# Performance work log

Measured on AMD Instinct MI355X. Metric: run time of the kernel, lower is better.

Reference implementation:

```python
import jax, jax.numpy as jnp
import numpy as np

D = 1024      # d_model
H = 16        # n_heads
HD = D // H   # head_dim = 64
B = 2
NQ = 2048     # prod(spatial_shape_q)
NK = 2048     # prod(spatial_shape_kv)
SCALE_BASE_Q = 2 * NQ   # spatial_shape_q[0] * 2
SCALE_BASE_K = 2 * NK   # spatial_shape_kv[0] * 2
THETA = 10000.0         # theta_rescale_factor=1.0 -> theta unchanged


def _init_freqs(dim):
    # learned_freq=True: parameter initialized to standard rotary frequencies
    return 1.0 / (THETA ** (jnp.arange(0, dim, 2, dtype=jnp.float32) / dim))


def _rotate_half(x):
    # interleaved pair rotation: (x1, x2) -> (-x2, x1)
    x1 = x[..., ::2]
    x2 = x[..., 1::2]
    return jnp.stack((-x2, x1), axis=-1).reshape(x.shape)


def _apply_rope_xpos(x, freqs_param, scale_base, sign):
    # x: (B, H, N, HD); freqs_param: (HD//2,)
    n = x.shape[2]
    dim = x.shape[-1]
    t = jnp.arange(n, dtype=jnp.float32)
    freqs = jnp.repeat(t[:, None] * freqs_param[None, :], 2, axis=-1)  # (N, HD)
    # xpos length-extrapolatable scaling
    power = (t - n // 2) / scale_base                                   # (N,)
    sv = (jnp.arange(0, dim, 2, dtype=jnp.float32) + 0.4 * dim) / (1.4 * dim)
    scale = jnp.repeat(sv[None, :] ** power[:, None], 2, axis=-1) ** sign  # (N, HD)
    return x * jnp.cos(freqs) * scale + _rotate_half(x) * jnp.sin(freqs) * scale


def setup_inputs() -> dict:
    key = jax.random.key(0)
    ks = jax.random.split(key, 10)
    s = 0.02
    return {
        "q_seq": jax.random.normal(ks[0], (B, NQ, D), jnp.float32),
        "kv_seq": jax.random.normal(ks[1], (B, NK, D), jnp.float32),
        "Wq": jax.random.normal(ks[2], (D, D), jnp.float32) * s,
        "bq": jnp.zeros((D,), jnp.float32),
        "Wk": jax.random.normal(ks[3], (D, D), jnp.float32) * s,
        "bk": jnp.zeros((D,), jnp.float32),
        "Wv": jax.random.normal(ks[4], (D, D), jnp.float32) * s,
        "bv": jnp.zeros((D,), jnp.float32),
        "Wo": jax.random.normal(ks[5], (D, D), jnp.float32) * s,
        "bo": jnp.zeros((D,), jnp.float32),
        "freqs_q": _init_freqs(HD),
        "freqs_kv": _init_freqs(HD),
    }


def reference(q_seq, kv_seq, Wq, bq, Wk, bk, Wv, bv, Wo, bo, freqs_q, freqs_kv):
    Bq, Nq, C = q_seq.shape
    Nk = kv_seq.shape[1]
    q = (q_seq @ Wq.T + bq).reshape(Bq, Nq, H, HD).transpose(0, 2, 1, 3)
    k = (kv_seq @ Wk.T + bk).reshape(Bq, Nk, H, HD).transpose(0, 2, 1, 3)
    v = (kv_seq @ Wv.T + bv).reshape(Bq, Nk, H, HD).transpose(0, 2, 1, 3)
    q = _apply_rope_xpos(q, freqs_q, SCALE_BASE_Q, sign=1.0)   # queries: scale^{+1}
    k = _apply_rope_xpos(k, freqs_kv, SCALE_BASE_K, sign=-1.0)  # keys: scale^{-1}
    attn = jax.nn.softmax(
        jnp.einsum("bhqd,bhkd->bhqk", q, k) * (HD ** -0.5), axis=-1
    )
    out = jnp.einsum("bhqk,bhkd->bhqd", attn, v)
    out = out.transpose(0, 2, 1, 3).reshape(Bq, Nq, C)
    return (out @ Wo.T + bo, attn)
```

## Files before the change

### kernel.cpp

```cpp
#include <hip/hip_runtime.h>

#define NQ 2048
#define NKK 2048
#define DD 1024
#define HH 16

typedef __attribute__((ext_vector_type(8))) short bf16x8;
typedef __attribute__((ext_vector_type(4))) float f32x4;

__device__ __forceinline__ short f2bf(float f){
    union { float f; unsigned u; } v; v.f = f;
    unsigned u = v.u + 0x7FFFu + ((v.u >> 16) & 1u);
    return (short)(u >> 16);
}
__device__ __forceinline__ float bf2f(unsigned short u){
    union { unsigned u; float f; } v; v.u = ((unsigned)u) << 16;
    return v.f;
}

__device__ __forceinline__ void gload16(const void* g, void* l){
    __builtin_amdgcn_global_load_lds(
        (__attribute__((address_space(1))) void*)g,
        (__attribute__((address_space(3))) void*)l,
        16, 0, 0);
}

__global__ __launch_bounds__(256) void cvt_bf16(const float* __restrict__ src,
                                                short* __restrict__ dst, int n){
    int i = (blockIdx.x * 256 + threadIdx.x) * 4;
    if (i < n){
        float4 v = *(const float4*)(src + i);
        union { short s[4]; uint2 u; } o;
        o.s[0] = f2bf(v.x); o.s[1] = f2bf(v.y);
        o.s[2] = f2bf(v.z); o.s[3] = f2bf(v.w);
        *(uint2*)(dst + i) = o.u;
    }
}

__global__ __launch_bounds__(256) void rope_kernel(const short* __restrict__ x,
                                                   short* __restrict__ y,
                                                   const float* __restrict__ fr,
                                                   int N, float scale_base,
                                                   float sign, float prescale){
    int p = blockIdx.x * 256 + threadIdx.x;
    int col2 = p & 511;
    int row  = p >> 9;
    int n    = row & (N - 1);
    int i    = col2 & 31;
    float t  = (float)n;
    float fv = t * fr[i];
    float c = cosf(fv), s = sinf(fv);
    float power = (t - (float)(N / 2)) / scale_base;
    float sv = ((float)(2 * i) + 0.4f * 64.f) / (1.4f * 64.f);
    float scale = exp2f(sign * power * log2f(sv)) * prescale;
    unsigned xv = *(const unsigned*)(x + 2 * (size_t)p);
    float x0 = bf2f((unsigned short)(xv & 0xFFFFu));
    float x1 = bf2f((unsigned short)(xv >> 16));
    float y0 = (x0 * c - x1 * s) * scale;
    float y1 = (x1 * c + x0 * s) * scale;
    unsigned o = (unsigned)(unsigned short)f2bf(y0) |
                 ((unsigned)(unsigned short)f2bf(y1) << 16);
    *(unsigned*)(y + 2 * (size_t)p) = o;
}

template<bool F32OUT>
__global__ __launch_bounds__(256) void gemm_bt(const short* __restrict__ A,
                                               const short* __restrict__ W,
                                               const float* __restrict__ bias,
                                               void* __restrict__ Cout,
                                               int M, int N, int K){
    __shared__ __align__(16) short lA[2][128 * 64];
    __shared__ __align__(16) short lB[2][128 * 64];
    int tid = threadIdx.x;
    int wave = tid >> 6, lane = tid & 63;
    int l16 = lane & 15, quad = lane >> 4;
    int wr = wave >> 1, wc = wave & 1;
    int row0 = blockIdx.y * 128, col0 = blockIdx.x * 128;

    const short* Ab = A + (size_t)(row0 + wave * 32 + (lane >> 3)) * K + (lane & 7) * 8;
    const short* Wb = W + (size_t)(col0 + wave * 32 + (lane >> 3)) * K + (lane & 7) * 8;

    f32x4 acc[4][4];
#pragma unroll
    for (int a = 0; a < 4; a++)
#pragma unroll
        for (int b = 0; b < 4; b++) acc[a][b] = (f32x4){0.f, 0.f, 0.f, 0.f};

    int nt = K >> 6;
#pragma unroll
    for (int i = 0; i < 4; i++){
        gload16(Ab + (size_t)i * 8 * K, &lA[0][(wave * 32 + i * 8) * 64]);
        gload16(Wb + (size_t)i * 8 * K, &lB[0][(wave * 32 + i * 8) * 64]);
    }
    __syncthreads();

    for (int t = 0; t < nt; t++){
        int cur = t & 1;
        if (t + 1 < nt){
            int k0 = (t + 1) << 6;
#pragma unroll
            for (int i = 0; i < 4; i++){
                gload16(Ab + (size_t)i * 8 * K + k0, &lA[cur ^ 1][(wave * 32 + i * 8) * 64]);
                gload16(Wb + (size_t)i * 8 * K + k0, &lB[cur ^ 1][(wave * 32 + i * 8) * 64]);
            }
        }
#pragma unroll
        for (int kk = 0; kk < 2; kk++){
            bf16x8 af[4], bfr[4];
#pragma unroll
            for (int t4 = 0; t4 < 4; t4++){
                af[t4]  = *(const bf16x8*)&lA[cur][(wr * 64 + t4 * 16 + l16) * 64 + kk * 32 + quad * 8];
                bfr[t4] = *(const bf16x8*)&lB[cur][(wc * 64 + t4 * 16 + l16) * 64 + kk * 32 + quad * 8];
            }
#pragma unroll
            for (int tm = 0; tm < 4; tm++)
#pragma unroll
                for (int tn = 0; tn < 4; tn++)
                    acc[tm][tn] = __builtin_amdgcn_mfma_f32_16x16x32_bf16(af[tm], bfr[tn], acc[tm][tn], 0, 0, 0);
        }
        __syncthreads();
    }

#pragma unroll
    for (int tm = 0; tm < 4; tm++){
        int gr = row0 + wr * 64 + tm * 16 + quad * 4;
#pragma unroll
        for (int tn = 0; tn < 4; tn++){
            int gc = col0 + wc * 64 + tn * 16 + l16;
            float bv = bias[gc];
#pragma unroll
            for (int r = 0; r < 4; r++){
                float v = acc[tm][tn][r] + bv;
                if (F32OUT) ((float*)Cout)[(size_t)(gr + r) * N + gc] = v;
                else        ((short*)Cout)[(size_t)(gr + r) * N + gc] = f2bf(v);
            }
        }
    }
}

__global__ __launch_bounds__(256) void transpose_v(const short* __restrict__ vp,
                                                   short* __restrict__ vT){
    __shared__ __align__(16) short tl[64 * 66];
    int kt = blockIdx.x;
    int bh = blockIdx.y;
    int b = bh >> 4, h = bh & 15;
    int tid = threadIdx.x;
    const short* src = vp + ((size_t)(b * NKK + kt * 64)) * DD + h * 64;
#pragma unroll
    for (int rd = 0; rd < 2; rd++){
        int kl = (tid >> 3) + rd * 32, c8 = (tid & 7) * 8;
        *(uint4*)&tl[kl * 66 + c8] = *(const uint4*)(src + (size_t)kl * DD + c8);
    }
    __syncthreads();
    short* dst = vT + ((size_t)(bh * 64)) * NKK + kt * 64;
#pragma unroll
    for (int rd = 0; rd < 2; rd++){
        int hd = (tid >> 3) + rd * 32, k8 = (tid & 7) * 8;
        union { short s[8]; uint4 u; } o;
#pragma unroll
        for (int j = 0; j < 8; j++) o.s[j] = tl[(k8 + j) * 66 + hd];
        *(uint4*)(dst + (size_t)hd * NKK + k8) = o.u;
    }
}

__global__ __launch_bounds__(256, 4) void attn_kernel(const short* __restrict__ qp,
                                                      const short* __restrict__ kp,
                                                      const short* __restrict__ vT,
                                                      float* __restrict__ attn,
                                                      short* __restrict__ op){
    __shared__ __align__(16) short lK[64 * 64];
    __shared__ __align__(16) short lV[64 * 64];
    __shared__ __align__(16) float lPf[64 * 68];
    __shared__ float lMf[64], lLi[64];

    int qt = blockIdx.x;
    int bh = blockIdx.y;
    int b = bh >> 4, h = bh & 15;
    int tid = threadIdx.x, wave = tid >> 6, lane = tid & 63;
    int l16 = lane & 15, quad = lane >> 4;

    int q0 = qt * 64;
    int qrow = q0 + wave * 16 + l16;
    const short* qb = qp + ((size_t)(b * NQ + qrow)) * DD + h * 64;
    bf16x8 qf[2];
    qf[0] = *(const bf16x8*)(qb + quad * 8);
    qf[1] = *(const bf16x8*)(qb + 32 + quad * 8);

    const short* kb = kp + ((size_t)(b * NKK)) * DD + h * 64;
    const short* vb = vT + ((size_t)(bh * 64)) * NKK;

    float m = -1e30f, l = 0.f;
    for (int kt = 0; kt < 32; kt++){
#pragma unroll
        for (int i = 0; i < 2; i++)
            gload16(kb + (size_t)(kt * 64 + wave * 16 + i * 8 + (lane >> 3)) * DD + (lane & 7) * 8,
                    &lK[(wave * 16 + i * 8) * 64]);
        __syncthreads();
        f32x4 St[4];
#pragma unroll
        for (int t = 0; t < 4; t++){
            f32x4 a = (f32x4){0.f, 0.f, 0.f, 0.f};
#pragma unroll
            for (int kk = 0; kk < 2; kk++){
                bf16x8 kf = *(const bf16x8*)&lK[(t * 16 + l16) * 64 + kk * 32 + quad * 8];
                a = __builtin_amdgcn_mfma_f32_16x16x32_bf16(kf, qf[kk], a, 0, 0, 0);
            }
            St[t] = a;
        }
        float mx = m;
#pragma unroll
        for (int t = 0; t < 4; t++)
#pragma unroll
            for (int r = 0; r < 4; r++) mx = fmaxf(mx, St[t][r]);
        float sum = 0.f;
#pragma unroll
        for (int t = 0; t < 4; t++)
#pragma unroll
            for (int r = 0; r < 4; r++) sum += __expf(St[t][r] - mx);
        l = l * __expf(m - mx) + sum;
        m = mx;
        __syncthreads();
    }
    float M = fmaxf(m, __shfl_xor(m, 16, 64));
    M = fmaxf(M, __shfl_xor(M, 32, 64));
    float ls = l * __expf(m - M);
    ls += __shfl_xor(ls, 16, 64);
    ls += __shfl_xor(ls, 32, 64);
    if (quad == 0){ lMf[wave * 16 + l16] = M; lLi[wave * 16 + l16] = 1.f / ls; }
    __syncthreads();
    float mf[4], il[4];
#pragma unroll
    for (int r = 0; r < 4; r++){
        mf[r] = lMf[wave * 16 + quad * 4 + r];
        il[r] = lLi[wave * 16 + quad * 4 + r];
    }

    f32x4 O[4];
#pragma unroll
    for (int th = 0; th < 4; th++) O[th] = (f32x4){0.f, 0.f, 0.f, 0.f};
    float* ab = attn + (((size_t)bh * NQ) + q0 + wave * 16) * NKK;

    for (int kt = 0; kt < 32; kt++){
#pragma unroll
        for (int i = 0; i < 2; i++){
            gload16(kb + (size_t)(kt * 64 + wave * 16 + i * 8 + (lane >> 3)) * DD + (lane & 7) * 8,
                    &lK[(wave * 16 + i * 8) * 64]);
            gload16(vb + (size_t)(wave * 16 + i * 8 + (lane >> 3)) * NKK + kt * 64 + (lane & 7) * 8,
                    &lV[(wave * 16 + i * 8) * 64]);
        }
        __syncthreads();
        f32x4 S[4];
#pragma unroll
        for (int tn = 0; tn < 4; tn++){
            f32x4 a = (f32x4){0.f, 0.f, 0.f, 0.f};
#pragma unroll
            for (int kk = 0; kk < 2; kk++){
                bf16x8 kf = *(const bf16x8*)&lK[(tn * 16 + l16) * 64 + kk * 32 + quad * 8];
                a = __builtin_amdgcn_mfma_f32_16x16x32_bf16(qf[kk], kf, a, 0, 0, 0);
            }
            S[tn] = a;
        }
#pragma unroll
        for (int tn = 0; tn < 4; tn++)
#pragma unroll
            for (int r = 0; r < 4; r++)
                lPf[(wave * 16 + quad * 4 + r) * 68 + tn * 16 + l16] =
                    __expf(S[tn][r] - mf[r]) * il[r];
#pragma unroll
        for (int j = 0; j < 4; j++){
            f32x4 pv = *(const f32x4*)&lPf[(wave * 16 + j * 4 + quad) * 68 + l16 * 4];
            __builtin_nontemporal_store(pv,
                (f32x4*)&ab[(size_t)(j * 4 + quad) * NKK + kt * 64 + l16 * 4]);
        }
#pragma unroll
        for (int kk = 0; kk < 2; kk++){
            f32x4 p0 = *(const f32x4*)&lPf[(wave * 16 + l16) * 68 + kk * 32 + quad * 8];
            f32x4 p1 = *(const f32x4*)&lPf[(wave * 16 + l16) * 68 + kk * 32 + quad * 8 + 4];
            union { short s[8]; bf16x8 v; } pf;
#pragma unroll
            for (int r = 0; r < 4; r++){ pf.s[r] = f2bf(p0[r]); pf.s[4 + r] = f2bf(p1[r]); }
#pragma unroll
            for (int th = 0; th < 4; th++){
                bf16x8 vf = *(const bf16x8*)&lV[(th * 16 + l16) * 64 + kk * 32 + quad * 8];
                O[th] = __builtin_amdgcn_mfma_f32_16x16x32_bf16(pf.v, vf, O[th], 0, 0, 0);
            }
        }
        __syncthreads();
    }
#pragma unroll
    for (int th = 0; th < 4; th++){
#pragma unroll
        for (int r = 0; r < 4; r++){
            int q = q0 + wave * 16 + quad * 4 + r;
            op[((size_t)(b * NQ + q)) * DD + h * 64 + th * 16 + l16] = f2bf(O[th][r]);
        }
    }
}

extern "C" void kernel_launch(void* const* d_in, const int* in_sizes, int n_in,
                              void* d_out, int out_size, void* d_ws, size_t ws_size,
                              hipStream_t stream) {
    const float* q_seq = (const float*)d_in[0];
    const float* kv_seq = (const float*)d_in[1];
    const float* Wq = (const float*)d_in[2];
    const float* bq = (const float*)d_in[3];
    const float* Wk = (const float*)d_in[4];
    const float* bk = (const float*)d_in[5];
    const float* Wv = (const float*)d_in[6];
    const float* bv = (const float*)d_in[7];
    const float* Wo = (const float*)d_in[8];
    const float* bo = (const float*)d_in[9];
    const float* freqs_q = (const float*)d_in[10];
    const float* freqs_kv = (const float*)d_in[11];

    float* out0 = (float*)d_out;
    float* attn = (float*)d_out + 4194304;

    short* qb  = (short*)d_ws;
    short* kvb = qb  + 4194304;
    short* wqb = kvb + 4194304;
    short* wkb = wqb + 1048576;
    short* wvb = wkb + 1048576;
    short* wob = wvb + 1048576;
    short* tmp = wob + 1048576;
    short* qpb = tmp + 4194304;
    short* kpb = qpb + 4194304;
    short* vpb = kpb + 4194304;
    short* vTb = qb;
    short* opb = tmp;

    cvt_bf16<<<4096, 256, 0, stream>>>(q_seq, qb, 4194304);
    cvt_bf16<<<4096, 256, 0, stream>>>(kv_seq, kvb, 4194304);
    cvt_bf16<<<1024, 256, 0, stream>>>(Wq, wqb, 1048576);
    cvt_bf16<<<1024, 256, 0, stream>>>(Wk, wkb, 1048576);
    cvt_bf16<<<1024, 256, 0, stream>>>(Wv, wvb, 1048576);
    cvt_bf16<<<1024, 256, 0, stream>>>(Wo, wob, 1048576);

    dim3 ggrid(8, 32);
    gemm_bt<false><<<ggrid, 256, 0, stream>>>(qb, wqb, bq, tmp, 4096, 1024, 1024);
    rope_kernel<<<8192, 256, 0, stream>>>(tmp, qpb, freqs_q, NQ, 4096.f, 1.f, 0.125f);
    gemm_bt<false><<<ggrid, 256, 0, stream>>>(kvb, wkb, bk, tmp, 4096, 1024, 1024);
    rope_kernel<<<8192, 256, 0, stream>>>(tmp, kpb, freqs_kv, NKK, 4096.f, -1.f, 1.f);
    gemm_bt<false><<<ggrid, 256, 0, stream>>>(kvb, wvb, bv, vpb, 4096, 1024, 1024);
    transpose_v<<<dim3(32, 32), 256, 0, stream>>>(vpb, vTb);
    attn_kernel<<<dim3(32, 32), 256, 0, stream>>>(qpb, kpb, vTb, attn, opb);
    gemm_bt<true><<<ggrid, 256, 0, stream>>>(opb, wob, bo, out0, 4096, 1024, 1024);
}
```

Before: 754.4 us.

## Fuse conversions, QKV projections with RoPE epilogue, and double-buffer attention tiles

Replaces six conversion launches with one kernel, precomputes RoPE cos/sin-scale tables, and fuses the Q/K/V projection GEMMs into one launch. That launch applies RoPE in the epilogue and writes V already transposed, removing the separate rope and transpose kernels and their intermediate buffers. The attention kernel double-buffers its K/V LDS tiles so the next tile is prefetched during compute, and it remaps blocks so each XCD works on the same heads. The extra LDS lowers occupancy to three blocks per CU, and the transposed V stores are 8-byte scattered writes.

```diff
diff --git a/kernel.cpp b/kernel.cpp
--- a/kernel.cpp
+++ b/kernel.cpp
@@ -25,42 +25,141 @@
         16, 0, 0);
 }
 
-__global__ __launch_bounds__(256) void cvt_bf16(const float* __restrict__ src,
-                                                short* __restrict__ dst, int n){
-    int i = (blockIdx.x * 256 + threadIdx.x) * 4;
-    if (i < n){
-        float4 v = *(const float4*)(src + i);
-        union { short s[4]; uint2 u; } o;
-        o.s[0] = f2bf(v.x); o.s[1] = f2bf(v.y);
-        o.s[2] = f2bf(v.z); o.s[3] = f2bf(v.w);
-        *(uint2*)(dst + i) = o.u;
-    }
-}
-
-__global__ __launch_bounds__(256) void rope_kernel(const short* __restrict__ x,
-                                                   short* __restrict__ y,
-                                                   const float* __restrict__ fr,
-                                                   int N, float scale_base,
-                                                   float sign, float prescale){
-    int p = blockIdx.x * 256 + threadIdx.x;
-    int col2 = p & 511;
-    int row  = p >> 9;
-    int n    = row & (N - 1);
-    int i    = col2 & 31;
-    float t  = (float)n;
-    float fv = t * fr[i];
-    float c = cosf(fv), s = sinf(fv);
-    float power = (t - (float)(N / 2)) / scale_base;
+__global__ __launch_bounds__(256) void cvt_all(
+    const float* __restrict__ q, const float* __restrict__ kv,
+    const float* __restrict__ wq, const float* __restrict__ wk,
+    const float* __restrict__ wv, const float* __restrict__ wo,
+    short* __restrict__ qb, short* __restrict__ kvb,
+    short* __restrict__ wqb, short* __restrict__ wkb,
+    short* __restrict__ wvb, short* __restrict__ wob){
+    int b = blockIdx.x;
+    const float* src; short* dst; int off;
+    if      (b < 4096) { src = q;  dst = qb;  off = b; }
+    else if (b < 8192) { src = kv; dst = kvb; off = b - 4096; }
+    else if (b < 9216) { src = wq; dst = wqb; off = b - 8192; }
+    else if (b < 10240){ src = wk; dst = wkb; off = b - 9216; }
+    else if (b < 11264){ src = wv; dst = wvb; off = b - 10240; }
+    else               { src = wo; dst = wob; off = b - 11264; }
+    int i = (off * 256 + threadIdx.x) * 4;
+    float4 v = *(const float4*)(src + i);
+    union { short s[4]; uint2 u; } o;
+    o.s[0] = f2bf(v.x); o.s[1] = f2bf(v.y);
+    o.s[2] = f2bf(v.z); o.s[3] = f2bf(v.w);
+    *(uint2*)(dst + i) = o.u;
+}
+
+__global__ __launch_bounds__(256) void rope_tables(
+    const float* __restrict__ frq, const float* __restrict__ frk,
+    float2* __restrict__ tq, float2* __restrict__ tk){
+    int idx = blockIdx.x * 256 + threadIdx.x;
+    int n = idx >> 5, i = idx & 31;
+    float t = (float)n;
+    float power = (t - 1024.f) / 4096.f;
     float sv = ((float)(2 * i) + 0.4f * 64.f) / (1.4f * 64.f);
-    float scale = exp2f(sign * power * log2f(sv)) * prescale;
-    unsigned xv = *(const unsigned*)(x + 2 * (size_t)p);
-    float x0 = bf2f((unsigned short)(xv & 0xFFFFu));
-    float x1 = bf2f((unsigned short)(xv >> 16));
-    float y0 = (x0 * c - x1 * s) * scale;
-    float y1 = (x1 * c + x0 * s) * scale;
-    unsigned o = (unsigned)(unsigned short)f2bf(y0) |
-                 ((unsigned)(unsigned short)f2bf(y1) << 16);
-    *(unsigned*)(y + 2 * (size_t)p) = o;
+    float lg = log2f(sv);
+    float scq = exp2f(power * lg) * 0.125f;
+    float sck = exp2f(-power * lg);
+    float fq = t * frq[i], fk = t * frk[i];
+    tq[idx] = make_float2(cosf(fq) * scq, sinf(fq) * scq);
+    tk[idx] = make_float2(cosf(fk) * sck, sinf(fk) * sck);
+}
+
+__global__ __launch_bounds__(256, 3) void proj_fused(
+    const short* __restrict__ qb, const short* __restrict__ kvb,
+    const short* __restrict__ wqb, const short* __restrict__ wkb,
+    const short* __restrict__ wvb,
+    const float* __restrict__ bq, const float* __restrict__ bk,
+    const float* __restrict__ bv,
+    const float2* __restrict__ tq, const float2* __restrict__ tk,
+    short* __restrict__ qpb, short* __restrict__ kpb,
+    short* __restrict__ vTb){
+    __shared__ __align__(16) short lA[128 * 64];
+    __shared__ __align__(16) short lB[128 * 64];
+    int bx = blockIdx.x;
+    int sec = bx >> 3, bxx = bx & 7;
+    const short* A = (sec == 0) ? qb : kvb;
+    const short* W = (sec == 0) ? wqb : (sec == 1 ? wkb : wvb);
+    const float* bias = (sec == 0) ? bq : (sec == 1 ? bk : bv);
+    const int K = 1024;
+    int tid = threadIdx.x;
+    int wave = tid >> 6, lane = tid & 63;
+    int l16 = lane & 15, quad = lane >> 4;
+    int wr = wave >> 1, wc = wave & 1;
+    int row0 = blockIdx.y * 128, col0 = bxx * 128;
+
+    const short* Ab = A + (size_t)(row0 + wave * 32 + (lane >> 3)) * K + (lane & 7) * 8;
+    const short* Wb = W + (size_t)(col0 + wave * 32 + (lane >> 3)) * K + (lane & 7) * 8;
+
+    f32x4 acc[4][4];
+#pragma unroll
+    for (int a = 0; a < 4; a++)
+#pragma unroll
+        for (int b = 0; b < 4; b++) acc[a][b] = (f32x4){0.f, 0.f, 0.f, 0.f};
+
+    for (int k0 = 0; k0 < K; k0 += 64){
+#pragma unroll
+        for (int i = 0; i < 4; i++){
+            gload16(Ab + (size_t)i * 8 * K + k0, &lA[(wave * 32 + i * 8) * 64]);
+            gload16(Wb + (size_t)i * 8 * K + k0, &lB[(wave * 32 + i * 8) * 64]);
+        }
+        __syncthreads();
+#pragma unroll
+        for (int kk = 0; kk < 2; kk++){
+            bf16x8 af[4], bfr[4];
+#pragma unroll
+            for (int t4 = 0; t4 < 4; t4++){
+                af[t4]  = *(const bf16x8*)&lA[(wr * 64 + t4 * 16 + l16) * 64 + kk * 32 + quad * 8];
+                bfr[t4] = *(const bf16x8*)&lB[(wc * 64 + t4 * 16 + l16) * 64 + kk * 32 + quad * 8];
+            }
+#pragma unroll
+            for (int tm = 0; tm < 4; tm++)
+#pragma unroll
+                for (int tn = 0; tn < 4; tn++)
+                    acc[tm][tn] = __builtin_amdgcn_mfma_f32_16x16x32_bf16(af[tm], bfr[tn], acc[tm][tn], 0, 0, 0);
+        }
+        __syncthreads();
+    }
+
+    if (sec == 2){
+#pragma unroll
+        for (int tm = 0; tm < 4; tm++){
+            int gr = row0 + wr * 64 + tm * 16 + quad * 4;
+            int b = gr >> 11, k = gr & 2047;
+#pragma unroll
+            for (int tn = 0; tn < 4; tn++){
+                int gc = col0 + wc * 64 + tn * 16 + l16;
+                int h = gc >> 6, hd = gc & 63;
+                float bvv = bias[gc];
+                union { short s[4]; uint2 u; } o;
+#pragma unroll
+                for (int r = 0; r < 4; r++) o.s[r] = f2bf(acc[tm][tn][r] + bvv);
+                *(uint2*)&vTb[((size_t)((b * 16 + h) * 64 + hd)) * 2048 + k] = o.u;
+            }
+        }
+    } else {
+        const float2* tbl = sec ? tk : tq;
+        short* outp = sec ? kpb : qpb;
+#pragma unroll
+        for (int tm = 0; tm < 4; tm++){
+#pragma unroll
+            for (int tn = 0; tn < 4; tn++){
+                int gc = col0 + wc * 64 + tn * 16 + l16;
+                int fi = (tn * 16 + l16) >> 1;
+                float sgn = (l16 & 1) ? 1.f : -1.f;
+                float bvv = bias[gc];
+#pragma unroll
+                for (int r = 0; r < 4; r++){
+                    int gr = row0 + wr * 64 + tm * 16 + quad * 4 + r;
+                    int n = gr & 2047;
+                    float v = acc[tm][tn][r] + bvv;
+                    float vp = __shfl_xor(v, 1, 64);
+                    float2 cs = tbl[n * 32 + fi];
+                    float y = v * cs.x + sgn * vp * cs.y;
+                    outp[(size_t)gr * 1024 + gc] = f2bf(y);
+                }
+            }
+        }
+    }
 }
 
 template<bool F32OUT>
@@ -138,43 +237,20 @@
     }
 }
 
-__global__ __launch_bounds__(256) void transpose_v(const short* __restrict__ vp,
-                                                   short* __restrict__ vT){
-    __shared__ __align__(16) short tl[64 * 66];
-    int kt = blockIdx.x;
-    int bh = blockIdx.y;
-    int b = bh >> 4, h = bh & 15;
-    int tid = threadIdx.x;
-    const short* src = vp + ((size_t)(b * NKK + kt * 64)) * DD + h * 64;
-#pragma unroll
-    for (int rd = 0; rd < 2; rd++){
-        int kl = (tid >> 3) + rd * 32, c8 = (tid & 7) * 8;
-        *(uint4*)&tl[kl * 66 + c8] = *(const uint4*)(src + (size_t)kl * DD + c8);
-    }
-    __syncthreads();
-    short* dst = vT + ((size_t)(bh * 64)) * NKK + kt * 64;
-#pragma unroll
-    for (int rd = 0; rd < 2; rd++){
-        int hd = (tid >> 3) + rd * 32, k8 = (tid & 7) * 8;
-        union { short s[8]; uint4 u; } o;
-#pragma unroll
-        for (int j = 0; j < 8; j++) o.s[j] = tl[(k8 + j) * 66 + hd];
-        *(uint4*)(dst + (size_t)hd * NKK + k8) = o.u;
-    }
-}
-
-__global__ __launch_bounds__(256, 4) void attn_kernel(const short* __restrict__ qp,
+__global__ __launch_bounds__(256, 3) void attn_kernel(const short* __restrict__ qp,
                                                       const short* __restrict__ kp,
                                                       const short* __restrict__ vT,
                                                       float* __restrict__ attn,
                                                       short* __restrict__ op){
-    __shared__ __align__(16) short lK[64 * 64];
-    __shared__ __align__(16) short lV[64 * 64];
+    __shared__ __align__(16) short lK[2][64 * 64];
+    __shared__ __align__(16) short lV[2][64 * 64];
     __shared__ __align__(16) float lPf[64 * 68];
     __shared__ float lMf[64], lLi[64];
 
-    int qt = blockIdx.x;
-    int bh = blockIdx.y;
+    int flat = blockIdx.y * 32 + blockIdx.x;
+    int xcd = flat & 7, idx = flat >> 3;
+    int qt = idx & 31;
+    int bh = xcd + 8 * (idx >> 5);
     int b = bh >> 4, h = bh & 15;
     int tid = threadIdx.x, wave = tid >> 6, lane = tid & 63;
     int l16 = lane & 15, quad = lane >> 4;
@@ -189,20 +265,30 @@
     const short* kb = kp + ((size_t)(b * NKK)) * DD + h * 64;
     const short* vb = vT + ((size_t)(bh * 64)) * NKK;
 
+#define STAGE_K(kt, buf) \
+    { _Pragma("unroll") \
+      for (int i = 0; i < 2; i++) \
+          gload16(kb + (size_t)((kt) * 64 + wave * 16 + i * 8 + (lane >> 3)) * DD + (lane & 7) * 8, \
+                  &lK[buf][(wave * 16 + i * 8) * 64]); }
+#define STAGE_V(kt, buf) \
+    { _Pragma("unroll") \
+      for (int i = 0; i < 2; i++) \
+          gload16(vb + (size_t)(wave * 16 + i * 8 + (lane >> 3)) * NKK + (kt) * 64 + (lane & 7) * 8, \
+                  &lV[buf][(wave * 16 + i * 8) * 64]); }
+
     float m = -1e30f, l = 0.f;
+    STAGE_K(0, 0);
+    __syncthreads();
     for (int kt = 0; kt < 32; kt++){
-#pragma unroll
-        for (int i = 0; i < 2; i++)
-            gload16(kb + (size_t)(kt * 64 + wave * 16 + i * 8 + (lane >> 3)) * DD + (lane & 7) * 8,
-                    &lK[(wave * 16 + i * 8) * 64]);
-        __syncthreads();
+        int cur = kt & 1;
+        if (kt < 31) STAGE_K(kt + 1, cur ^ 1);
         f32x4 St[4];
 #pragma unroll
         for (int t = 0; t < 4; t++){
             f32x4 a = (f32x4){0.f, 0.f, 0.f, 0.f};
 #pragma unroll
             for (int kk = 0; kk < 2; kk++){
-                bf16x8 kf = *(const bf16x8*)&lK[(t * 16 + l16) * 64 + kk * 32 + quad * 8];
+                bf16x8 kf = *(const bf16x8*)&lK[cur][(t * 16 + l16) * 64 + kk * 32 + quad * 8];
                 a = __builtin_amdgcn_mfma_f32_16x16x32_bf16(kf, qf[kk], a, 0, 0, 0);
             }
             St[t] = a;
@@ -240,22 +326,19 @@
     for (int th = 0; th < 4; th++) O[th] = (f32x4){0.f, 0.f, 0.f, 0.f};
     float* ab = attn + (((size_t)bh * NQ) + q0 + wave * 16) * NKK;
 
+    STAGE_K(0, 0);
+    STAGE_V(0, 0);
+    __syncthreads();
     for (int kt = 0; kt < 32; kt++){
-#pragma unroll
-        for (int i = 0; i < 2; i++){
-            gload16(kb + (size_t)(kt * 64 + wave * 16 + i * 8 + (lane >> 3)) * DD + (lane & 7) * 8,
-                    &lK[(wave * 16 + i * 8) * 64]);
-            gload16(vb + (size_t)(wave * 16 + i * 8 + (lane >> 3)) * NKK + kt * 64 + (lane & 7) * 8,
-                    &lV[(wave * 16 + i * 8) * 64]);
-        }
-        __syncthreads();
+        int cur = kt & 1;
+        if (kt < 31){ STAGE_K(kt + 1, cur ^ 1); STAGE_V(kt + 1, cur ^ 1); }
         f32x4 S[4];
 #pragma unroll
         for (int tn = 0; tn < 4; tn++){
             f32x4 a = (f32x4){0.f, 0.f, 0.f, 0.f};
 #pragma unroll
             for (int kk = 0; kk < 2; kk++){
-                bf16x8 kf = *(const bf16x8*)&lK[(tn * 16 + l16) * 64 + kk * 32 + quad * 8];
+                bf16x8 kf = *(const bf16x8*)&lK[cur][(tn * 16 + l16) * 64 + kk * 32 + quad * 8];
                 a = __builtin_amdgcn_mfma_f32_16x16x32_bf16(qf[kk], kf, a, 0, 0, 0);
             }
             S[tn] = a;
@@ -281,7 +364,7 @@
             for (int r = 0; r < 4; r++){ pf.s[r] = f2bf(p0[r]); pf.s[4 + r] = f2bf(p1[r]); }
 #pragma unroll
             for (int th = 0; th < 4; th++){
-                bf16x8 vf = *(const bf16x8*)&lV[(th * 16 + l16) * 64 + kk * 32 + quad * 8];
+                bf16x8 vf = *(const bf16x8*)&lV[cur][(th * 16 + l16) * 64 + kk * 32 + quad * 8];
                 O[th] = __builtin_amdgcn_mfma_f32_16x16x32_bf16(pf.v, vf, O[th], 0, 0, 0);
             }
         }
@@ -295,6 +378,8 @@
             op[((size_t)(b * NQ + q)) * DD + h * 64 + th * 16 + l16] = f2bf(O[th][r]);
         }
     }
+#undef STAGE_K
+#undef STAGE_V
 }
 
 extern "C" void kernel_launch(void* const* d_in, const int* in_sizes, int n_in,
@@ -322,27 +407,19 @@
     short* wkb = wqb + 1048576;
     short* wvb = wkb + 1048576;
     short* wob = wvb + 1048576;
-    short* tmp = wob + 1048576;
-    short* qpb = tmp + 4194304;
+    short* qpb = wob + 1048576;
     short* kpb = qpb + 4194304;
-    short* vpb = kpb + 4194304;
-    short* vTb = qb;
-    short* opb = tmp;
-
-    cvt_bf16<<<4096, 256, 0, stream>>>(q_seq, qb, 4194304);
-    cvt_bf16<<<4096, 256, 0, stream>>>(kv_seq, kvb, 4194304);
-    cvt_bf16<<<1024, 256, 0, stream>>>(Wq, wqb, 1048576);
-    cvt_bf16<<<1024, 256, 0, stream>>>(Wk, wkb, 1048576);
-    cvt_bf16<<<1024, 256, 0, stream>>>(Wv, wvb, 1048576);
-    cvt_bf16<<<1024, 256, 0, stream>>>(Wo, wob, 1048576);
-
-    dim3 ggrid(8, 32);
-    gemm_bt<false><<<ggrid, 256, 0, stream>>>(qb, wqb, bq, tmp, 4096, 1024, 1024);
-    rope_kernel<<<8192, 256, 0, stream>>>(tmp, qpb, freqs_q, NQ, 4096.f, 1.f, 0.125f);
-    gemm_bt<false><<<ggrid, 256, 0, stream>>>(kvb, wkb, bk, tmp, 4096, 1024, 1024);
-    rope_kernel<<<8192, 256, 0, stream>>>(tmp, kpb, freqs_kv, NKK, 4096.f, -1.f, 1.f);
-    gemm_bt<false><<<ggrid, 256, 0, stream>>>(kvb, wvb, bv, vpb, 4096, 1024, 1024);
-    transpose_v<<<dim3(32, 32), 256, 0, stream>>>(vpb, vTb);
+    short* vTb = kpb + 4194304;
+    float2* tq = (float2*)(vTb + 4194304);
+    float2* tk = tq + 65536;
+    short* opb = qb;
+
+    cvt_all<<<12288, 256, 0, stream>>>(q_seq, kv_seq, Wq, Wk, Wv, Wo,
+                                       qb, kvb, wqb, wkb, wvb, wob);
+    rope_tables<<<256, 256, 0, stream>>>(freqs_q, freqs_kv, tq, tk);
+    proj_fused<<<dim3(24, 32), 256, 0, stream>>>(qb, kvb, wqb, wkb, wvb,
+                                                 bq, bk, bv, tq, tk,
+                                                 qpb, kpb, vTb);
     attn_kernel<<<dim3(32, 32), 256, 0, stream>>>(qpb, kpb, vTb, attn, opb);
-    gemm_bt<true><<<ggrid, 256, 0, stream>>>(opb, wob, bo, out0, 4096, 1024, 1024);
-}
+    gemm_bt<true><<<dim3(8, 32), 256, 0, stream>>>(opb, wob, bo, out0, 4096, 1024, 1024);
+}
```

Measured after the change: 719.0 us. 1.05x faster.
